# Performance work log

Hardware: AMD Instinct MI355X
Metric: run time of the kernel (lower is better)

## Reference

```python
import jax, jax.numpy as jnp
import numpy as np

B, F, L = 256, 32, 4096  # batch, num_filters, length == input_dim


def setup_inputs() -> dict:
    key = jax.random.key(0)
    k1, k2, k3 = jax.random.split(key, 3)
    x = jax.random.normal(k1, (B, L), dtype=jnp.float32)
    window_params = jax.random.normal(k2, (F, L), dtype=jnp.float32) * 0.02
    # original init: linspace(0.1, 0.5, F).unsqueeze(0); use same deterministic init
    freq_params = jnp.linspace(0.1, 0.5, F, dtype=jnp.float32)[None, :]
    return {"x": x, "window_params": window_params, "freq_params": freq_params}


def reference(x, window_params, freq_params):
    # x: [B, L]; window_params: [F, L]; freq_params: [1, F]
    length = x.shape[-1]
    windows = jax.nn.softmax(window_params, axis=-1)            # [F, L]
    freqs = jax.nn.sigmoid(freq_params)[0] * 0.5                # [F]
    n = jnp.arange(length, dtype=jnp.float32)                   # [L]
    # complex modulation atoms for ALL filters at once (single batched FFT)
    phase = -2.0 * jnp.pi * freqs[:, None] * n[None, :]         # [F, L]
    modulation = jnp.exp(1j * phase.astype(jnp.complex64))      # [F, L] complex64
    atoms = windows.astype(jnp.complex64) * modulation          # [F, L]
    Xf = jnp.fft.fft(x, axis=-1)                                # [B, L]
    Af = jnp.fft.fft(atoms, axis=-1)                            # [F, L]
    # circular correlation of x with each atom, all filters batched
    prod = Xf[:, None, :] * jnp.conj(Af)[None, :, :]            # [B, F, L]
    return jnp.real(jnp.fft.ifft(prod, axis=-1)).astype(x.dtype)  # [B, F, L]
```

## Files before the change

### kernel.cpp

```cpp
#include <hip/hip_runtime.h>
#include <math.h>

#define B 256
#define F 32
#define L 4096
#define NT 256
#define TWO_PI 6.28318530717958647692f

__device__ __forceinline__ int pidx(int i) { return i + (i >> 4); }

__device__ __forceinline__ int rev3(int i) {
    return ((i & 15) << 8) | (i & 0xF0) | (i >> 8);
}

__device__ __forceinline__ float2 cmul(float2 a, float2 b) {
    return make_float2(a.x * b.x - a.y * b.y, a.x * b.y + a.y * b.x);
}
__device__ __forceinline__ float2 cmulc(float2 a, float cr, float ci) {
    return make_float2(a.x * cr - a.y * ci, a.x * ci + a.y * cr);
}

template<int SGN>
__device__ __forceinline__ void dft4(float2& a, float2& b, float2& c, float2& d) {
    const float s = (float)SGN;
    float2 t0 = make_float2(a.x + c.x, a.y + c.y);
    float2 t1 = make_float2(a.x - c.x, a.y - c.y);
    float2 t2 = make_float2(b.x + d.x, b.y + d.y);
    float2 t3 = make_float2(b.x - d.x, b.y - d.y);
    float2 it3 = make_float2(-s * t3.y, s * t3.x);
    a = make_float2(t0.x + t2.x, t0.y + t2.y);
    c = make_float2(t0.x - t2.x, t0.y - t2.y);
    b = make_float2(t1.x + it3.x, t1.y + it3.y);
    d = make_float2(t1.x - it3.x, t1.y - it3.y);
}

template<int SGN>
__device__ __forceinline__ void dft16(float2 v[16]) {
    const float s = (float)SGN;
    const float C1 = 0.92387953251128675613f;
    const float S1 = 0.38268343236508977173f;
    const float C2 = 0.70710678118654752440f;
    #pragma unroll
    for (int c = 0; c < 4; ++c) dft4<SGN>(v[c], v[c + 4], v[c + 8], v[c + 12]);
    v[5]  = cmulc(v[5],  C1,  s * S1);
    v[6]  = cmulc(v[6],  C2,  s * C2);
    v[7]  = cmulc(v[7],  S1,  s * C1);
    v[9]  = cmulc(v[9],  C2,  s * C2);
    v[10] = make_float2(-s * v[10].y, s * v[10].x);
    v[11] = cmulc(v[11], -C2, s * C2);
    v[13] = cmulc(v[13], S1,  s * C1);
    v[14] = cmulc(v[14], -C2, s * C2);
    v[15] = cmulc(v[15], -C1, -s * S1);
    float2 o[16];
    #pragma unroll
    for (int m = 0; m < 4; ++m) {
        float2 a = v[4*m], b = v[4*m+1], c = v[4*m+2], d = v[4*m+3];
        dft4<SGN>(a, b, c, d);
        o[m] = a; o[m+4] = b; o[m+8] = c; o[m+12] = d;
    }
    #pragma unroll
    for (int i = 0; i < 16; ++i) v[i] = o[i];
}

__device__ __forceinline__ void twiddle_pow(float2 v[16], float2 w1) {
    float2 w = w1;
    #pragma unroll
    for (int q = 1; q < 16; ++q) {
        v[q] = cmul(v[q], w);
        w = cmul(w, w1);
    }
}

template<int SGN>
__device__ __forceinline__ void gen_tw(int t, float2& w1, float2& u1) {
    float sv, cv;
    sincosf((float)SGN * (TWO_PI / (float)L) * (float)t, &sv, &cv);
    w1 = make_float2(cv, sv);
    sincosf((float)SGN * (TWO_PI / 256.0f) * (float)(t & 15), &sv, &cv);
    u1 = make_float2(cv, sv);
}

__device__ __forceinline__ void fft_dif_fwd(float2 v[16], float2* lds, int t) {
    float2 w1, u1;
    gen_tw<-1>(t, w1, u1);
    dft16<-1>(v);
    twiddle_pow(v, w1);
    #pragma unroll
    for (int p = 0; p < 16; ++p) lds[pidx(t + 256 * p)] = v[p];
    __syncthreads();
    const int base = (t >> 4) * 256 + (t & 15);
    #pragma unroll
    for (int q = 0; q < 16; ++q) v[q] = lds[pidx(base + 16 * q)];
    dft16<-1>(v);
    twiddle_pow(v, u1);
    #pragma unroll
    for (int p = 0; p < 16; ++p) lds[pidx(base + 16 * p)] = v[p];
    #pragma unroll
    for (int q = 0; q < 16; ++q) v[q] = lds[pidx(16 * t + q)];
    dft16<-1>(v);
}

__global__ void __launch_bounds__(NT) prep_kernel(const float* __restrict__ x,
                                                  const float* __restrict__ wp,
                                                  const float* __restrict__ fp,
                                                  float2* __restrict__ Znat,
                                                  float2* __restrict__ Anat) {
    __shared__ float2 lds[L + (L >> 4)];
    __shared__ float red[4];
    const int t = threadIdx.x;
    float2 v[16];

    if (blockIdx.x < F) {
        const int f = blockIdx.x;
        const float* row = wp + (size_t)f * L;
        float rv[16];
        #pragma unroll
        for (int c = 0; c < 16; ++c) rv[c] = row[t + 256 * c];
        float m = -INFINITY;
        #pragma unroll
        for (int c = 0; c < 16; ++c) m = fmaxf(m, rv[c]);
        #pragma unroll
        for (int off = 32; off; off >>= 1) m = fmaxf(m, __shfl_down(m, off));
        if ((t & 63) == 0) red[t >> 6] = m;
        __syncthreads();
        m = fmaxf(fmaxf(red[0], red[1]), fmaxf(red[2], red[3]));
        __syncthreads();
        float s = 0.0f;
        #pragma unroll
        for (int c = 0; c < 16; ++c) { rv[c] = expf(rv[c] - m); s += rv[c]; }
        #pragma unroll
        for (int off = 32; off; off >>= 1) s += __shfl_down(s, off);
        if ((t & 63) == 0) red[t >> 6] = s;
        __syncthreads();
        s = red[0] + red[1] + red[2] + red[3];
        const float inv = 1.0f / s;
        const float fr = 0.5f / (1.0f + expf(-fp[f]));
        const float w0 = -TWO_PI * fr;
        #pragma unroll
        for (int c = 0; c < 16; ++c) {
            const int n = t + 256 * c;
            const float e = rv[c] * inv;
            float sv, cv;
            sincosf(w0 * (float)n, &sv, &cv);
            v[c] = make_float2(e * cv, e * sv);
        }
        fft_dif_fwd(v, lds, t);
        float2* an = Anat + (size_t)f * L;
        #pragma unroll
        for (int r = 0; r < 16; ++r) an[rev3(16 * t + r)] = v[r];
    } else {
        const int m = blockIdx.x - F;
        const float* r0 = x + (size_t)(2 * m) * L;
        const float* r1 = r0 + L;
        #pragma unroll
        for (int q = 0; q < 16; ++q)
            v[q] = make_float2(r0[t + 256 * q], r1[t + 256 * q]);
        fft_dif_fwd(v, lds, t);
        float2* zn = Znat + (size_t)m * L;
        #pragma unroll
        for (int r = 0; r < 16; ++r) zn[rev3(16 * t + r)] = v[r];
    }
}

__global__ void __launch_bounds__(NT) pair_kernel(const float2* __restrict__ Anat,
                                                  const float2* __restrict__ Znat,
                                                  float2* __restrict__ Cs,
                                                  float2* __restrict__ Xs) {
    const int t = threadIdx.x;
    if (blockIdx.x < (F / 2)) {
        const int j = blockIdx.x;
        const float2* a0 = Anat + (size_t)(2 * j) * L;
        const float2* a1 = a0 + L;
        const float sc = 0.5f / (float)L;
        float2* co = Cs + (size_t)j * L;
        #pragma unroll
        for (int c = 0; c < 16; ++c) {
            const int i = t + 256 * c;
            const int k = rev3(i);
            const int km = (L - k) & (L - 1);
            const float2 a0k = a0[k], a0m = a0[km];
            const float2 a1k = a1[k], a1m = a1[km];
            const float g0r = a0k.x + a0m.x, g0i = a0m.y - a0k.y;
            const float g1r = a1k.x + a1m.x, g1i = a1m.y - a1k.y;
            co[i] = make_float2((g0r - g1i) * sc, (g0i + g1r) * sc);
        }
    } else {
        const int m = blockIdx.x - (F / 2);
        const float2* z = Znat + (size_t)m * L;
        float2* o0 = Xs + (size_t)(2 * m) * L;
        float2* o1 = o0 + L;
        #pragma unroll
        for (int c = 0; c < 16; ++c) {
            const int i = t + 256 * c;
            const int k = rev3(i);
            const int km = (L - k) & (L - 1);
            const float2 zk = z[k], zm = z[km];
            o0[i] = make_float2(0.5f * (zk.x + zm.x), 0.5f * (zk.y - zm.y));
            o1[i] = make_float2(0.5f * (zk.y + zm.y), 0.5f * (zm.x - zk.x));
        }
    }
}

__global__ void __launch_bounds__(NT, 4) corr_kernel(const float2* __restrict__ Xs,
                                                     const float2* __restrict__ Cs,
                                                     float* __restrict__ out) {
    __shared__ float2 lds[L + (L >> 4)];
    const int blk = blockIdx.x;
    const int jf = (blk >> 3) & 15;
    const int b = ((blk >> 7) << 3) | (blk & 7);
    const int t = threadIdx.x;

    const float4* x4 = (const float4*)(Xs + (size_t)b * L + 16 * t);
    const float4* c4 = (const float4*)(Cs + (size_t)jf * L + 16 * t);
    float4 xa[8], ca[8];
    #pragma unroll
    for (int h = 0; h < 8; ++h) { xa[h] = x4[h]; ca[h] = c4[h]; }

    float2 w1, u1;
    gen_tw<1>(t, w1, u1);

    float2 v[16];
    #pragma unroll
    for (int h = 0; h < 8; ++h) {
        v[2*h]   = cmul(make_float2(xa[h].x, xa[h].y), make_float2(ca[h].x, ca[h].y));
        v[2*h+1] = cmul(make_float2(xa[h].z, xa[h].w), make_float2(ca[h].z, ca[h].w));
    }
    dft16<1>(v);
    #pragma unroll
    for (int r = 0; r < 16; ++r) lds[pidx(16 * t + r)] = v[r];
    const int base = (t >> 4) * 256 + (t & 15);
    #pragma unroll
    for (int q = 0; q < 16; ++q) v[q] = lds[pidx(base + 16 * q)];
    twiddle_pow(v, u1);
    dft16<1>(v);
    #pragma unroll
    for (int r = 0; r < 16; ++r) lds[pidx(base + 16 * r)] = v[r];
    __syncthreads();
    #pragma unroll
    for (int q = 0; q < 16; ++q) v[q] = lds[pidx(t + 256 * q)];
    twiddle_pow(v, w1);
    dft16<1>(v);
    float* o0 = out + ((size_t)b * F + 2 * jf) * L;
    float* o1 = o0 + L;
    #pragma unroll
    for (int r = 0; r < 16; ++r) {
        __builtin_nontemporal_store(v[r].x, o0 + t + 256 * r);
        __builtin_nontemporal_store(v[r].y, o1 + t + 256 * r);
    }
}

extern "C" void kernel_launch(void* const* d_in, const int* in_sizes, int n_in,
                              void* d_out, int out_size, void* d_ws, size_t ws_size,
                              hipStream_t stream) {
    (void)in_sizes; (void)n_in; (void)out_size; (void)ws_size;
    const float* x  = (const float*)d_in[0];
    const float* wp = (const float*)d_in[1];
    const float* fp = (const float*)d_in[2];
    float* out = (float*)d_out;

    float2* Xs   = (float2*)d_ws;
    float2* Cs   = Xs + (size_t)B * L;
    float2* Anat = Cs + (size_t)(F / 2) * L;
    float2* Znat = Anat + (size_t)F * L;

    prep_kernel<<<dim3(F + B / 2), dim3(NT), 0, stream>>>(x, wp, fp, Znat, Anat);
    pair_kernel<<<dim3(F / 2 + B / 2), dim3(NT), 0, stream>>>(Anat, Znat, Cs, Xs);
    corr_kernel<<<dim3(B * F / 2), dim3(NT), 0, stream>>>(Xs, Cs, out);
}
```

Baseline: 182.6 us.

## Fuse prep and pair kernels via LDS spectra and use LDS twiddle table

Merges the FFT prep kernel and the conjugate-symmetry pair kernel into one launch. Each block keeps its spectra in swizzled shared memory rather than round-tripping them through global memory, and atom blocks now compute two atom FFTs each. In corr_kernel, the per-thread twiddle power generation for the middle stage is replaced by a shared 16x17 twiddle table filled with one sincos per thread. The cost is much larger LDS use in prep (about 100KB per block), which lowers occupancy, plus an extra barrier in corr.

```diff
diff --git a/kernel.cpp b/kernel.cpp
--- a/kernel.cpp
+++ b/kernel.cpp
@@ -11,6 +11,10 @@
 
 __device__ __forceinline__ int rev3(int i) {
     return ((i & 15) << 8) | (i & 0xF0) | (i >> 8);
+}
+
+__device__ __forceinline__ int sw(int a) {
+    return a ^ ((a >> 4) & 15) ^ ((a >> 8) & 15);
 }
 
 __device__ __forceinline__ float2 cmul(float2 a, float2 b) {
@@ -100,77 +104,65 @@
     dft16<-1>(v);
 }
 
+__device__ __forceinline__ void atom_fft(const float* __restrict__ row, float fpv,
+                                         float2 v[16], float2* lds, float* red, int t) {
+    float rv[16];
+    #pragma unroll
+    for (int c = 0; c < 16; ++c) rv[c] = row[t + 256 * c];
+    float m = -INFINITY;
+    #pragma unroll
+    for (int c = 0; c < 16; ++c) m = fmaxf(m, rv[c]);
+    #pragma unroll
+    for (int off = 32; off; off >>= 1) m = fmaxf(m, __shfl_down(m, off));
+    if ((t & 63) == 0) red[t >> 6] = m;
+    __syncthreads();
+    m = fmaxf(fmaxf(red[0], red[1]), fmaxf(red[2], red[3]));
+    __syncthreads();
+    float s = 0.0f;
+    #pragma unroll
+    for (int c = 0; c < 16; ++c) { rv[c] = expf(rv[c] - m); s += rv[c]; }
+    #pragma unroll
+    for (int off = 32; off; off >>= 1) s += __shfl_down(s, off);
+    if ((t & 63) == 0) red[t >> 6] = s;
+    __syncthreads();
+    s = red[0] + red[1] + red[2] + red[3];
+    const float inv = 1.0f / s;
+    const float fr = 0.5f / (1.0f + expf(-fpv));
+    const float w0 = -TWO_PI * fr;
+    #pragma unroll
+    for (int c = 0; c < 16; ++c) {
+        const int n = t + 256 * c;
+        const float e = rv[c] * inv;
+        float sv, cv;
+        sincosf(w0 * (float)n, &sv, &cv);
+        v[c] = make_float2(e * cv, e * sv);
+    }
+    __syncthreads();
+    fft_dif_fwd(v, lds, t);
+}
+
 __global__ void __launch_bounds__(NT) prep_kernel(const float* __restrict__ x,
                                                   const float* __restrict__ wp,
                                                   const float* __restrict__ fp,
-                                                  float2* __restrict__ Znat,
-                                                  float2* __restrict__ Anat) {
+                                                  float2* __restrict__ Cs,
+                                                  float2* __restrict__ Xs) {
     __shared__ float2 lds[L + (L >> 4)];
+    __shared__ float2 specA[L];
+    __shared__ float2 specB[L];
     __shared__ float red[4];
     const int t = threadIdx.x;
     float2 v[16];
 
-    if (blockIdx.x < F) {
-        const int f = blockIdx.x;
-        const float* row = wp + (size_t)f * L;
-        float rv[16];
-        #pragma unroll
-        for (int c = 0; c < 16; ++c) rv[c] = row[t + 256 * c];
-        float m = -INFINITY;
-        #pragma unroll
-        for (int c = 0; c < 16; ++c) m = fmaxf(m, rv[c]);
-        #pragma unroll
-        for (int off = 32; off; off >>= 1) m = fmaxf(m, __shfl_down(m, off));
-        if ((t & 63) == 0) red[t >> 6] = m;
-        __syncthreads();
-        m = fmaxf(fmaxf(red[0], red[1]), fmaxf(red[2], red[3]));
-        __syncthreads();
-        float s = 0.0f;
-        #pragma unroll
-        for (int c = 0; c < 16; ++c) { rv[c] = expf(rv[c] - m); s += rv[c]; }
-        #pragma unroll
-        for (int off = 32; off; off >>= 1) s += __shfl_down(s, off);
-        if ((t & 63) == 0) red[t >> 6] = s;
-        __syncthreads();
-        s = red[0] + red[1] + red[2] + red[3];
-        const float inv = 1.0f / s;
-        const float fr = 0.5f / (1.0f + expf(-fp[f]));
-        const float w0 = -TWO_PI * fr;
-        #pragma unroll
-        for (int c = 0; c < 16; ++c) {
-            const int n = t + 256 * c;
-            const float e = rv[c] * inv;
-            float sv, cv;
-            sincosf(w0 * (float)n, &sv, &cv);
-            v[c] = make_float2(e * cv, e * sv);
-        }
-        fft_dif_fwd(v, lds, t);
-        float2* an = Anat + (size_t)f * L;
-        #pragma unroll
-        for (int r = 0; r < 16; ++r) an[rev3(16 * t + r)] = v[r];
-    } else {
-        const int m = blockIdx.x - F;
-        const float* r0 = x + (size_t)(2 * m) * L;
-        const float* r1 = r0 + L;
-        #pragma unroll
-        for (int q = 0; q < 16; ++q)
-            v[q] = make_float2(r0[t + 256 * q], r1[t + 256 * q]);
-        fft_dif_fwd(v, lds, t);
-        float2* zn = Znat + (size_t)m * L;
-        #pragma unroll
-        for (int r = 0; r < 16; ++r) zn[rev3(16 * t + r)] = v[r];
-    }
-}
-
-__global__ void __launch_bounds__(NT) pair_kernel(const float2* __restrict__ Anat,
-                                                  const float2* __restrict__ Znat,
-                                                  float2* __restrict__ Cs,
-                                                  float2* __restrict__ Xs) {
-    const int t = threadIdx.x;
     if (blockIdx.x < (F / 2)) {
         const int j = blockIdx.x;
-        const float2* a0 = Anat + (size_t)(2 * j) * L;
-        const float2* a1 = a0 + L;
+        atom_fft(wp + (size_t)(2 * j) * L, fp[2 * j], v, lds, red, t);
+        #pragma unroll
+        for (int r = 0; r < 16; ++r) specA[sw(rev3(16 * t + r))] = v[r];
+        __syncthreads();
+        atom_fft(wp + (size_t)(2 * j + 1) * L, fp[2 * j + 1], v, lds, red, t);
+        #pragma unroll
+        for (int r = 0; r < 16; ++r) specB[sw(rev3(16 * t + r))] = v[r];
+        __syncthreads();
         const float sc = 0.5f / (float)L;
         float2* co = Cs + (size_t)j * L;
         #pragma unroll
@@ -178,15 +170,24 @@
             const int i = t + 256 * c;
             const int k = rev3(i);
             const int km = (L - k) & (L - 1);
-            const float2 a0k = a0[k], a0m = a0[km];
-            const float2 a1k = a1[k], a1m = a1[km];
+            const float2 a0k = specA[sw(k)], a0m = specA[sw(km)];
+            const float2 a1k = specB[sw(k)], a1m = specB[sw(km)];
             const float g0r = a0k.x + a0m.x, g0i = a0m.y - a0k.y;
             const float g1r = a1k.x + a1m.x, g1i = a1m.y - a1k.y;
             co[i] = make_float2((g0r - g1i) * sc, (g0i + g1r) * sc);
         }
     } else {
         const int m = blockIdx.x - (F / 2);
-        const float2* z = Znat + (size_t)m * L;
+        const float* r0 = x + (size_t)(2 * m) * L;
+        const float* r1 = r0 + L;
+        #pragma unroll
+        for (int q = 0; q < 16; ++q)
+            v[q] = make_float2(r0[t + 256 * q], r1[t + 256 * q]);
+        __syncthreads();
+        fft_dif_fwd(v, lds, t);
+        #pragma unroll
+        for (int r = 0; r < 16; ++r) specA[sw(rev3(16 * t + r))] = v[r];
+        __syncthreads();
         float2* o0 = Xs + (size_t)(2 * m) * L;
         float2* o1 = o0 + L;
         #pragma unroll
@@ -194,7 +195,7 @@
             const int i = t + 256 * c;
             const int k = rev3(i);
             const int km = (L - k) & (L - 1);
-            const float2 zk = z[k], zm = z[km];
+            const float2 zk = specA[sw(k)], zm = specA[sw(km)];
             o0[i] = make_float2(0.5f * (zk.x + zm.x), 0.5f * (zk.y - zm.y));
             o1[i] = make_float2(0.5f * (zk.y + zm.y), 0.5f * (zm.x - zk.x));
         }
@@ -205,6 +206,7 @@
                                                      const float2* __restrict__ Cs,
                                                      float* __restrict__ out) {
     __shared__ float2 lds[L + (L >> 4)];
+    __shared__ float2 T1[272];
     const int blk = blockIdx.x;
     const int jf = (blk >> 3) & 15;
     const int b = ((blk >> 7) << 3) | (blk & 7);
@@ -216,8 +218,13 @@
     #pragma unroll
     for (int h = 0; h < 8; ++h) { xa[h] = x4[h]; ca[h] = c4[h]; }
 
-    float2 w1, u1;
-    gen_tw<1>(t, w1, u1);
+    float sv, cv;
+    sincosf((TWO_PI / 256.0f) * (float)((t >> 4) * (t & 15)), &sv, &cv);
+    T1[17 * (t >> 4) + (t & 15)] = make_float2(cv, sv);
+    float2 w1;
+    sincosf((TWO_PI / (float)L) * (float)t, &sv, &cv);
+    w1 = make_float2(cv, sv);
+    __syncthreads();
 
     float2 v[16];
     #pragma unroll
@@ -231,7 +238,11 @@
     const int base = (t >> 4) * 256 + (t & 15);
     #pragma unroll
     for (int q = 0; q < 16; ++q) v[q] = lds[pidx(base + 16 * q)];
-    twiddle_pow(v, u1);
+    {
+        const float2* Tr = T1 + 17 * (t & 15);
+        #pragma unroll
+        for (int q = 1; q < 16; ++q) v[q] = cmul(v[q], Tr[q]);
+    }
     dft16<1>(v);
     #pragma unroll
     for (int r = 0; r < 16; ++r) lds[pidx(base + 16 * r)] = v[r];
@@ -258,12 +269,9 @@
     const float* fp = (const float*)d_in[2];
     float* out = (float*)d_out;
 
-    float2* Xs   = (float2*)d_ws;
-    float2* Cs   = Xs + (size_t)B * L;
-    float2* Anat = Cs + (size_t)(F / 2) * L;
-    float2* Znat = Anat + (size_t)F * L;
-
-    prep_kernel<<<dim3(F + B / 2), dim3(NT), 0, stream>>>(x, wp, fp, Znat, Anat);
-    pair_kernel<<<dim3(F / 2 + B / 2), dim3(NT), 0, stream>>>(Anat, Znat, Cs, Xs);
+    float2* Xs = (float2*)d_ws;
+    float2* Cs = Xs + (size_t)B * L;
+
+    prep_kernel<<<dim3(F / 2 + B / 2), dim3(NT), 0, stream>>>(x, wp, fp, Cs, Xs);
     corr_kernel<<<dim3(B * F / 2), dim3(NT), 0, stream>>>(Xs, Cs, out);
 }
```

Result: no change. 181.2 us (-0.8%).
